# Kernel optimization log

Measured on AMD Instinct MI355X. Metric: run time of the kernel, lower is better.

Reference implementation:

```python
import jax, jax.numpy as jnp
import numpy as np

EPS = 1e-8  # RMSNormMultiHead default eps (forward passes self.eps)


def rms_norm_multihead(x, weight):
    # x: (B, L, H, d); normalize over last dim in float32, then scale per (H, d)
    x32 = x.astype(jnp.float32)
    normed = x32 * jax.lax.rsqrt(jnp.mean(x32 * x32, axis=-1, keepdims=True) + EPS)
    return normed.astype(x.dtype) * weight


def setup_inputs() -> dict:
    key = jax.random.key(0)
    k0, k1, k2 = jax.random.split(key, 3)
    B, L, D, H = 2, 1024, 1024, 16
    d = D // H
    X = jax.random.normal(k0, (B, L, D), dtype=jnp.float32)
    Wq = jax.random.normal(k1, (D, D), dtype=jnp.float32) * 0.02  # q_proj weight (out, in)
    Wv = jax.random.normal(k2, (D, D), dtype=jnp.float32) * 0.02  # v_proj weight (out, in)
    q_norm_w = jnp.ones((H, d), dtype=jnp.float32)
    v_norm_w = jnp.ones((H, d), dtype=jnp.float32)
    return {"X": X, "Wq": Wq, "Wv": Wv, "q_norm_w": q_norm_w, "v_norm_w": v_norm_w}


def reference(X, Wq, Wv, q_norm_w, v_norm_w):
    B, L, D = X.shape
    H, d = q_norm_w.shape
    K = X.reshape(B, L, H, d)
    Q = rms_norm_multihead((X @ Wq.T).reshape(B, L, H, d), q_norm_w)
    V = rms_norm_multihead((X @ Wv.T).reshape(B, L, H, d), v_norm_w)
    # cumulative outer-product KV state: (B, L, H, d, e)
    W = jnp.cumsum(jnp.einsum('blhd,blhe->blhde', K, V), axis=1)
    out = jnp.einsum('blhd,blhde->blhe', Q, W).reshape(B, L, D)
    return out
```

## Files before the change

### kernel.cpp

```cpp
#include <hip/hip_runtime.h>

#define BB 2
#define LL 1024
#define DD 1024
#define HH 16
#define NC 16
#define EPSF 1e-8f

typedef __attribute__((ext_vector_type(8))) short bf16x8;
typedef __attribute__((ext_vector_type(4))) float f32x4;
typedef unsigned short u16;

static __device__ inline u16 f2bf(float f) {
    unsigned int u = __builtin_bit_cast(unsigned int, f);
    u += 0x7fff + ((u >> 16) & 1);
    return (u16)(u >> 16);
}

static __device__ inline void gload_lds16(const u16* g, u16* l) {
    __builtin_amdgcn_global_load_lds((const __attribute__((address_space(1))) void*)g,
                                     (__attribute__((address_space(3))) void*)l, 16, 0, 0);
}

__global__ __launch_bounds__(256) void cvt_k(const float* __restrict__ X,
                                             const float* __restrict__ Wq,
                                             const float* __restrict__ Wv,
                                             u16* __restrict__ Xb,
                                             u16* __restrict__ Wqb,
                                             u16* __restrict__ Wvb)
{
    int i = (blockIdx.x * 256 + threadIdx.x) * 4;
    const float* s; u16* d; int off;
    if (i < 2*1024*1024)      { s = X;  d = Xb;  off = i; }
    else if (i < 3*1024*1024) { s = Wq; d = Wqb; off = i - 2*1024*1024; }
    else                      { s = Wv; d = Wvb; off = i - 3*1024*1024; }
    float4 v = *(const float4*)(s + off);
    ushort4 o;
    o.x = f2bf(v.x); o.y = f2bf(v.y); o.z = f2bf(v.z); o.w = f2bf(v.w);
    *(ushort4*)(d + off) = o;
}

__global__ __launch_bounds__(256) void gemm_fused(const u16* __restrict__ Xb,
                                                  const u16* __restrict__ Wqb,
                                                  const u16* __restrict__ Wvb,
                                                  const float* __restrict__ qw,
                                                  const float* __restrict__ vw,
                                                  u16* __restrict__ Qb,
                                                  u16* __restrict__ Vb)
{
    const int K = DD, N = DD;
    const u16* W = blockIdx.z ? Wvb : Wqb;
    const float* nw = blockIdx.z ? vw : qw;
    u16* Y = blockIdx.z ? Vb : Qb;
    __shared__ u16 As0[128 * 32], As1[128 * 32];
    __shared__ u16 Bs0[64 * 32],  Bs1[64 * 32];

    const int tid = threadIdx.x, w = tid >> 6, lane = tid & 63;
    const int quad = lane >> 4, l16 = lane & 15;
    const int m0 = blockIdx.y * 128, n0 = blockIdx.x * 64;
    const int lrow = lane >> 2, lcol = (lane & 3) * 8;

    const u16* gA0 = Xb + (size_t)(m0 + w*16 + lrow) * K + lcol;
    const u16* gA1 = gA0 + (size_t)64 * K;
    const u16* gB0 = W + (size_t)(n0 + w*16 + lrow) * K + lcol;
    u16* lA0_0 = &As0[(w*16) * 32];      u16* lA0_1 = &As1[(w*16) * 32];
    u16* lA1_0 = &As0[(64 + w*16) * 32]; u16* lA1_1 = &As1[(64 + w*16) * 32];
    u16* lB0_0 = &Bs0[(w*16) * 32];      u16* lB0_1 = &Bs1[(w*16) * 32];

    f32x4 acc[2][4] = {};
    for (int k0 = 0; k0 < K; k0 += 64) {
        gload_lds16(gA0 + k0,      lA0_0);
        gload_lds16(gA0 + k0 + 32, lA0_1);
        gload_lds16(gA1 + k0,      lA1_0);
        gload_lds16(gA1 + k0 + 32, lA1_1);
        gload_lds16(gB0 + k0,      lB0_0);
        gload_lds16(gB0 + k0 + 32, lB0_1);
        __syncthreads();
        #pragma unroll
        for (int hh = 0; hh < 2; ++hh) {
            const u16* Ah = hh ? As1 : As0;
            const u16* Bh = hh ? Bs1 : Bs0;
            bf16x8 af[2], bfr[4];
            #pragma unroll
            for (int i = 0; i < 2; ++i)
                af[i] = *(const bf16x8*)&Ah[(w*32 + i*16 + l16) * 32 + quad*8];
            #pragma unroll
            for (int j = 0; j < 4; ++j)
                bfr[j] = *(const bf16x8*)&Bh[(j*16 + l16) * 32 + quad*8];
            #pragma unroll
            for (int i = 0; i < 2; ++i)
                #pragma unroll
                for (int j = 0; j < 4; ++j)
                    acc[i][j] = __builtin_amdgcn_mfma_f32_16x16x32_bf16(af[i], bfr[j], acc[i][j], 0, 0, 0);
        }
        __syncthreads();
    }

    float wv[4];
    #pragma unroll
    for (int j = 0; j < 4; ++j) wv[j] = nw[n0 + j*16 + l16];
    #pragma unroll
    for (int i = 0; i < 2; ++i) {
        float ss[4];
        #pragma unroll
        for (int r = 0; r < 4; ++r) {
            float s = 0.f;
            #pragma unroll
            for (int j = 0; j < 4; ++j) s += acc[i][j][r] * acc[i][j][r];
            ss[r] = s;
        }
        #pragma unroll
        for (int off = 1; off < 16; off <<= 1)
            #pragma unroll
            for (int r = 0; r < 4; ++r) ss[r] += __shfl_xor(ss[r], off, 64);
        float sc[4];
        #pragma unroll
        for (int r = 0; r < 4; ++r) sc[r] = rsqrtf(ss[r] * (1.f/64.f) + EPSF);
        #pragma unroll
        for (int r = 0; r < 4; ++r) {
            u16* yp = Y + (size_t)(m0 + w*32 + i*16 + quad*4 + r) * N + n0;
            #pragma unroll
            for (int j = 0; j < 4; ++j)
                yp[j*16 + l16] = f2bf(acc[i][j][r] * sc[r] * wv[j]);
        }
    }
}

__global__ __launch_bounds__(256) void kv_scan(const u16* __restrict__ Xb,
                                               const u16* __restrict__ Vb,
                                               u16* __restrict__ S)
{
    const int t = blockIdx.x & 3, bh = blockIdx.x >> 2;
    const int et = t & 1, dt = t >> 1;
    const int h = bh & 15, b = bh >> 4;
    __shared__ u16 Kt[2][32][72];
    __shared__ u16 Vt[2][32][72];
    const int tid = threadIdx.x, w = tid >> 6, lane = tid & 63;
    const int quad = lane >> 4, l16 = lane & 15;
    const int esub = (w & 1) * 16, dsub = (w >> 1) * 16;
    const int half = tid >> 7, hrow = (tid & 127) >> 1, hq = tid & 1;
    const u16* gsrc = (half ? Vb : Xb) + (size_t)(b*LL + hrow) * DD
                      + h*64 + (half ? et : dt) * 32 + hq*16;
    u16 (*Tb)[32][72] = half ? Vt : Kt;
    ushort4 rr[4];

    auto loadc = [&](int c) {
        const u16* p = gsrc + (size_t)c * 64 * DD;
        rr[0] = *(const ushort4*)(p);      rr[1] = *(const ushort4*)(p + 4);
        rr[2] = *(const ushort4*)(p + 8);  rr[3] = *(const ushort4*)(p + 12);
    };
    auto writec = [&](int buf) {
        #pragma unroll
        for (int i = 0; i < 16; ++i)
            Tb[buf][hq*16 + i][hrow] = ((const u16*)rr)[i];
    };

    loadc(0); writec(0); loadc(1);
    __syncthreads();
    f32x4 acc = {};
    for (int c = 0; c < NC; ++c) {
        const int cur = c & 1;
        if (c + 1 < NC) writec(1 - cur);
        if (c + 2 < NC) loadc(c + 2);
        u16* Sp = S + (((size_t)(bh*NC + c)) << 12) + t*1024 + w*256;
        #pragma unroll
        for (int r = 0; r < 4; ++r) Sp[r*64 + lane] = f2bf(acc[r]);
        #pragma unroll
        for (int k0 = 0; k0 < 64; k0 += 32) {
            bf16x8 av = *(const bf16x8*)&Vt[cur][esub + l16][k0 + quad*8];
            bf16x8 bv = *(const bf16x8*)&Kt[cur][dsub + l16][k0 + quad*8];
            acc = __builtin_amdgcn_mfma_f32_16x16x32_bf16(av, bv, acc, 0, 0, 0);
        }
        __syncthreads();
    }
}

__global__ __launch_bounds__(256) void out_k(const u16* __restrict__ Xb,
                                             const u16* __restrict__ Qb,
                                             const u16* __restrict__ Vb,
                                             const u16* __restrict__ S,
                                             float* __restrict__ out)
{
    const int c = blockIdx.x & 15, bh = blockIdx.x >> 4;
    const int h = bh & 15, b = bh >> 4;
    __shared__ u16 Qs[64][72];
    __shared__ u16 Ks[64][72];
    __shared__ u16 Vt[64][72];
    __shared__ u16 St[64][72];
    const int tid = threadIdx.x;
    {
        const int row = tid >> 2, q = tid & 3;
        size_t gbase = (size_t)(b*LL + c*64 + row) * DD + h*64 + q*16;
        u16 vv[16];
        #pragma unroll
        for (int i = 0; i < 16; i += 4) {
            *(ushort4*)&Qs[row][q*16 + i] = *(const ushort4*)(Qb + gbase + i);
            *(ushort4*)&Ks[row][q*16 + i] = *(const ushort4*)(Xb + gbase + i);
            *(ushort4*)&vv[i] = *(const ushort4*)(Vb + gbase + i);
        }
        #pragma unroll
        for (int i = 0; i < 16; ++i)
            Vt[q*16 + i][row] = vv[i];
        const u16* Sc = S + (((size_t)(bh*NC + c)) << 12);
        #pragma unroll
        for (int j = 0; j < 4; ++j) {
            int f = (tid + j*256) * 4;
            ushort4 sv = *(const ushort4*)(Sc + f);
            int tt = f >> 10, ww = (f >> 8) & 3, rr_ = (f >> 6) & 3, ln = f & 63;
            int e = (tt & 1)*32 + (ww & 1)*16 + (ln >> 4)*4 + rr_;
            int d = (tt >> 1)*32 + ((ww >> 1) & 1)*16 + (ln & 15);
            *(ushort4*)&St[e][d] = sv;
        }
    }
    __syncthreads();
    const int w = tid >> 6, lane = tid & 63, quad = lane >> 4, l16 = lane & 15;
    const int mo = (w & 1) * 32, no = (w >> 1) * 32;

    f32x4 pacc[2][2] = {};
    #pragma unroll
    for (int k0 = 0; k0 < 64; k0 += 32) {
        bf16x8 aq[2], bk[2];
        #pragma unroll
        for (int i = 0; i < 2; ++i)
            aq[i] = *(const bf16x8*)&Qs[mo + i*16 + l16][k0 + quad*8];
        #pragma unroll
        for (int j = 0; j < 2; ++j)
            bk[j] = *(const bf16x8*)&Ks[no + j*16 + l16][k0 + quad*8];
        #pragma unroll
        for (int i = 0; i < 2; ++i)
            #pragma unroll
            for (int j = 0; j < 2; ++j)
                pacc[i][j] = __builtin_amdgcn_mfma_f32_16x16x32_bf16(aq[i], bk[j], pacc[i][j], 0, 0, 0);
    }
    __syncthreads();
    #pragma unroll
    for (int i = 0; i < 2; ++i)
        #pragma unroll
        for (int j = 0; j < 2; ++j)
            #pragma unroll
            for (int r = 0; r < 4; ++r) {
                int l  = mo + i*16 + quad*4 + r;
                int lp = no + j*16 + l16;
                Ks[l][lp] = (lp <= l) ? f2bf(pacc[i][j][r]) : (u16)0;
            }
    __syncthreads();

    f32x4 acc[2][2] = {};
    #pragma unroll
    for (int k0 = 0; k0 < 64; k0 += 32) {
        bf16x8 a1[2], b1[2], a2[2], b2[2];
        #pragma unroll
        for (int i = 0; i < 2; ++i) {
            a1[i] = *(const bf16x8*)&Ks[mo + i*16 + l16][k0 + quad*8];
            a2[i] = *(const bf16x8*)&Qs[mo + i*16 + l16][k0 + quad*8];
        }
        #pragma unroll
        for (int j = 0; j < 2; ++j) {
            b1[j] = *(const bf16x8*)&Vt[no + j*16 + l16][k0 + quad*8];
            b2[j] = *(const bf16x8*)&St[no + j*16 + l16][k0 + quad*8];
        }
        #pragma unroll
        for (int i = 0; i < 2; ++i)
            #pragma unroll
            for (int j = 0; j < 2; ++j) {
                acc[i][j] = __builtin_amdgcn_mfma_f32_16x16x32_bf16(a1[i], b1[j], acc[i][j], 0, 0, 0);
                acc[i][j] = __builtin_amdgcn_mfma_f32_16x16x32_bf16(a2[i], b2[j], acc[i][j], 0, 0, 0);
            }
    }
    float* op = out + (size_t)(b*LL + c*64) * DD + h*64;
    #pragma unroll
    for (int i = 0; i < 2; ++i)
        #pragma unroll
        for (int j = 0; j < 2; ++j)
            #pragma unroll
            for (int r = 0; r < 4; ++r)
                op[(size_t)(mo + i*16 + quad*4 + r) * DD + no + j*16 + l16] = acc[i][j][r];
}

extern "C" void kernel_launch(void* const* d_in, const int* in_sizes, int n_in,
                              void* d_out, int out_size, void* d_ws, size_t ws_size,
                              hipStream_t stream) {
    const float* X  = (const float*)d_in[0];
    const float* Wq = (const float*)d_in[1];
    const float* Wv = (const float*)d_in[2];
    const float* qw = (const float*)d_in[3];
    const float* vw = (const float*)d_in[4];
    float* out = (float*)d_out;

    u16* Xb  = (u16*)d_ws;
    u16* Wqb = Xb  + (size_t)2*1024*1024;
    u16* Wvb = Wqb + (size_t)1024*1024;
    u16* Qb  = Wvb + (size_t)1024*1024;
    u16* Vb  = Qb  + (size_t)2*1024*1024;
    u16* S   = Vb  + (size_t)2*1024*1024;

    cvt_k<<<4096, 256, 0, stream>>>(X, Wq, Wv, Xb, Wqb, Wvb);
    gemm_fused<<<dim3(16, 16, 2), 256, 0, stream>>>(Xb, Wqb, Wvb, qw, vw, Qb, Vb);
    kv_scan<<<128, 256, 0, stream>>>(Xb, Vb, S);
    out_k<<<BB*HH*NC, 256, 0, stream>>>(Xb, Qb, Vb, S, out);
}
```

Before: 106.2 us.

## Fuse all stages into one cooperative persistent kernel with chunk-parallel KV scan

Replaces the four separate launches (convert, fused GEMM+RMSNorm, KV scan, output) with a single cooperative kernel of 512 blocks that separates the phases with grid.sync. The sequential per-head KV scan is restructured into chunk-local outer-product sums computed in parallel, followed by a separate exclusive prefix pass over the 16 chunks. This targets launch overhead and the serial dependency in the old 128-block scan. In exchange it pays for grid-wide barriers, an extra global read/write of the state buffer, and requires all 512 blocks to be co-resident.

```diff
diff --git a/kernel.cpp b/kernel.cpp
--- a/kernel.cpp
+++ b/kernel.cpp
@@ -1,4 +1,7 @@
 #include <hip/hip_runtime.h>
+#include <hip/hip_cooperative_groups.h>
+
+namespace cg = cooperative_groups;
 
 #define BB 2
 #define LL 1024
@@ -10,271 +13,287 @@
 typedef __attribute__((ext_vector_type(8))) short bf16x8;
 typedef __attribute__((ext_vector_type(4))) float f32x4;
 typedef unsigned short u16;
+typedef u16 (*tile_t)[72];
 
 static __device__ inline u16 f2bf(float f) {
     unsigned int u = __builtin_bit_cast(unsigned int, f);
     u += 0x7fff + ((u >> 16) & 1);
     return (u16)(u >> 16);
 }
-
+static __device__ inline float bf2f(u16 v) {
+    unsigned int u = ((unsigned int)v) << 16;
+    return __builtin_bit_cast(float, u);
+}
 static __device__ inline void gload_lds16(const u16* g, u16* l) {
     __builtin_amdgcn_global_load_lds((const __attribute__((address_space(1))) void*)g,
                                      (__attribute__((address_space(3))) void*)l, 16, 0, 0);
 }
 
-__global__ __launch_bounds__(256) void cvt_k(const float* __restrict__ X,
-                                             const float* __restrict__ Wq,
-                                             const float* __restrict__ Wv,
-                                             u16* __restrict__ Xb,
-                                             u16* __restrict__ Wqb,
-                                             u16* __restrict__ Wvb)
+__global__ __launch_bounds__(256, 2) void fused_all(
+    const float* __restrict__ X, const float* __restrict__ Wq,
+    const float* __restrict__ Wv, const float* __restrict__ qw,
+    const float* __restrict__ vw,
+    u16* __restrict__ Xb, u16* __restrict__ Wqb, u16* __restrict__ Wvb,
+    u16* __restrict__ Qb, u16* __restrict__ Vb, u16* __restrict__ S,
+    float* __restrict__ out)
 {
-    int i = (blockIdx.x * 256 + threadIdx.x) * 4;
-    const float* s; u16* d; int off;
-    if (i < 2*1024*1024)      { s = X;  d = Xb;  off = i; }
-    else if (i < 3*1024*1024) { s = Wq; d = Wqb; off = i - 2*1024*1024; }
-    else                      { s = Wv; d = Wvb; off = i - 3*1024*1024; }
-    float4 v = *(const float4*)(s + off);
-    ushort4 o;
-    o.x = f2bf(v.x); o.y = f2bf(v.y); o.z = f2bf(v.z); o.w = f2bf(v.w);
-    *(ushort4*)(d + off) = o;
-}
-
-__global__ __launch_bounds__(256) void gemm_fused(const u16* __restrict__ Xb,
-                                                  const u16* __restrict__ Wqb,
-                                                  const u16* __restrict__ Wvb,
-                                                  const float* __restrict__ qw,
-                                                  const float* __restrict__ vw,
-                                                  u16* __restrict__ Qb,
-                                                  u16* __restrict__ Vb)
-{
-    const int K = DD, N = DD;
-    const u16* W = blockIdx.z ? Wvb : Wqb;
-    const float* nw = blockIdx.z ? vw : qw;
-    u16* Y = blockIdx.z ? Vb : Qb;
-    __shared__ u16 As0[128 * 32], As1[128 * 32];
-    __shared__ u16 Bs0[64 * 32],  Bs1[64 * 32];
-
-    const int tid = threadIdx.x, w = tid >> 6, lane = tid & 63;
+    cg::grid_group grid = cg::this_grid();
+    __shared__ u16 smem[18432];
+
+    const int tid = threadIdx.x, bid = blockIdx.x;
+    const int w = tid >> 6, lane = tid & 63;
     const int quad = lane >> 4, l16 = lane & 15;
-    const int m0 = blockIdx.y * 128, n0 = blockIdx.x * 64;
-    const int lrow = lane >> 2, lcol = (lane & 3) * 8;
-
-    const u16* gA0 = Xb + (size_t)(m0 + w*16 + lrow) * K + lcol;
-    const u16* gA1 = gA0 + (size_t)64 * K;
-    const u16* gB0 = W + (size_t)(n0 + w*16 + lrow) * K + lcol;
-    u16* lA0_0 = &As0[(w*16) * 32];      u16* lA0_1 = &As1[(w*16) * 32];
-    u16* lA1_0 = &As0[(64 + w*16) * 32]; u16* lA1_1 = &As1[(64 + w*16) * 32];
-    u16* lB0_0 = &Bs0[(w*16) * 32];      u16* lB0_1 = &Bs1[(w*16) * 32];
-
-    f32x4 acc[2][4] = {};
-    for (int k0 = 0; k0 < K; k0 += 64) {
-        gload_lds16(gA0 + k0,      lA0_0);
-        gload_lds16(gA0 + k0 + 32, lA0_1);
-        gload_lds16(gA1 + k0,      lA1_0);
-        gload_lds16(gA1 + k0 + 32, lA1_1);
-        gload_lds16(gB0 + k0,      lB0_0);
-        gload_lds16(gB0 + k0 + 32, lB0_1);
+
+    {
+        int i0 = (bid * 256 + tid) * 4;
+        #pragma unroll
+        for (int p = 0; p < 8; ++p) {
+            int i = i0 + p * 524288;
+            const float* s; u16* d; int off;
+            if (i < 2*1024*1024)      { s = X;  d = Xb;  off = i; }
+            else if (i < 3*1024*1024) { s = Wq; d = Wqb; off = i - 2*1024*1024; }
+            else                      { s = Wv; d = Wvb; off = i - 3*1024*1024; }
+            float4 v = *(const float4*)(s + off);
+            ushort4 o;
+            o.x = f2bf(v.x); o.y = f2bf(v.y); o.z = f2bf(v.z); o.w = f2bf(v.w);
+            *(ushort4*)(d + off) = o;
+        }
+    }
+    grid.sync();
+
+    {
+        const int z = bid >> 8, rem = bid & 255;
+        const int n0 = (rem & 15) * 64, m0 = (rem >> 4) * 128;
+        const u16* Wb = z ? Wvb : Wqb;
+        const float* nw = z ? vw : qw;
+        u16* Y = z ? Vb : Qb;
+        u16* As0 = smem;
+        u16* As1 = smem + 4096;
+        u16* Bs0 = smem + 8192;
+        u16* Bs1 = smem + 10240;
+
+        const int lrow = lane >> 2, lcol = (lane & 3) * 8;
+        const u16* gA0 = Xb + (size_t)(m0 + w*16 + lrow) * DD + lcol;
+        const u16* gA1 = gA0 + (size_t)64 * DD;
+        const u16* gB0 = Wb + (size_t)(n0 + w*16 + lrow) * DD + lcol;
+        u16* lA0_0 = &As0[(w*16) * 32];      u16* lA0_1 = &As1[(w*16) * 32];
+        u16* lA1_0 = &As0[(64 + w*16) * 32]; u16* lA1_1 = &As1[(64 + w*16) * 32];
+        u16* lB0_0 = &Bs0[(w*16) * 32];      u16* lB0_1 = &Bs1[(w*16) * 32];
+
+        f32x4 acc[2][4] = {};
+        for (int k0 = 0; k0 < DD; k0 += 64) {
+            gload_lds16(gA0 + k0,      lA0_0);
+            gload_lds16(gA0 + k0 + 32, lA0_1);
+            gload_lds16(gA1 + k0,      lA1_0);
+            gload_lds16(gA1 + k0 + 32, lA1_1);
+            gload_lds16(gB0 + k0,      lB0_0);
+            gload_lds16(gB0 + k0 + 32, lB0_1);
+            __syncthreads();
+            #pragma unroll
+            for (int hh = 0; hh < 2; ++hh) {
+                const u16* Ah = hh ? As1 : As0;
+                const u16* Bh = hh ? Bs1 : Bs0;
+                bf16x8 af[2], bfr[4];
+                #pragma unroll
+                for (int i = 0; i < 2; ++i)
+                    af[i] = *(const bf16x8*)&Ah[(w*32 + i*16 + l16) * 32 + quad*8];
+                #pragma unroll
+                for (int j = 0; j < 4; ++j)
+                    bfr[j] = *(const bf16x8*)&Bh[(j*16 + l16) * 32 + quad*8];
+                #pragma unroll
+                for (int i = 0; i < 2; ++i)
+                    #pragma unroll
+                    for (int j = 0; j < 4; ++j)
+                        acc[i][j] = __builtin_amdgcn_mfma_f32_16x16x32_bf16(af[i], bfr[j], acc[i][j], 0, 0, 0);
+            }
+            __syncthreads();
+        }
+        float wv4[4];
+        #pragma unroll
+        for (int j = 0; j < 4; ++j) wv4[j] = nw[n0 + j*16 + l16];
+        #pragma unroll
+        for (int i = 0; i < 2; ++i) {
+            float ss[4];
+            #pragma unroll
+            for (int r = 0; r < 4; ++r) {
+                float s = 0.f;
+                #pragma unroll
+                for (int j = 0; j < 4; ++j) s += acc[i][j][r] * acc[i][j][r];
+                ss[r] = s;
+            }
+            #pragma unroll
+            for (int off = 1; off < 16; off <<= 1)
+                #pragma unroll
+                for (int r = 0; r < 4; ++r) ss[r] += __shfl_xor(ss[r], off, 64);
+            float sc[4];
+            #pragma unroll
+            for (int r = 0; r < 4; ++r) sc[r] = rsqrtf(ss[r] * (1.f/64.f) + EPSF);
+            #pragma unroll
+            for (int r = 0; r < 4; ++r) {
+                u16* yp = Y + (size_t)(m0 + w*32 + i*16 + quad*4 + r) * DD + n0;
+                #pragma unroll
+                for (int j = 0; j < 4; ++j)
+                    yp[j*16 + l16] = f2bf(acc[i][j][r] * sc[r] * wv4[j]);
+            }
+        }
+    }
+    grid.sync();
+
+    {
+        const int bh = bid >> 4, c = bid & 15;
+        const int h = bh & 15, b = bh >> 4;
+        tile_t Kt = (tile_t)smem;
+        tile_t Vt = (tile_t)(smem + 4608);
+        {
+            const int row = tid >> 2, q = tid & 3;
+            size_t gbase = (size_t)(b*LL + c*64 + row) * DD + h*64 + q*16;
+            u16 kk[16], vv[16];
+            #pragma unroll
+            for (int i = 0; i < 16; i += 4) {
+                *(ushort4*)&kk[i] = *(const ushort4*)(Xb + gbase + i);
+                *(ushort4*)&vv[i] = *(const ushort4*)(Vb + gbase + i);
+            }
+            #pragma unroll
+            for (int i = 0; i < 16; ++i) {
+                Kt[q*16 + i][row] = kk[i];
+                Vt[q*16 + i][row] = vv[i];
+            }
+        }
         __syncthreads();
-        #pragma unroll
-        for (int hh = 0; hh < 2; ++hh) {
-            const u16* Ah = hh ? As1 : As0;
-            const u16* Bh = hh ? Bs1 : Bs0;
-            bf16x8 af[2], bfr[4];
-            #pragma unroll
-            for (int i = 0; i < 2; ++i)
-                af[i] = *(const bf16x8*)&Ah[(w*32 + i*16 + l16) * 32 + quad*8];
-            #pragma unroll
-            for (int j = 0; j < 4; ++j)
-                bfr[j] = *(const bf16x8*)&Bh[(j*16 + l16) * 32 + quad*8];
-            #pragma unroll
-            for (int i = 0; i < 2; ++i)
-                #pragma unroll
-                for (int j = 0; j < 4; ++j)
-                    acc[i][j] = __builtin_amdgcn_mfma_f32_16x16x32_bf16(af[i], bfr[j], acc[i][j], 0, 0, 0);
+        const int me = (w & 1) * 32, nd = (w >> 1) * 32;
+        f32x4 acc[2][2] = {};
+        #pragma unroll
+        for (int k0 = 0; k0 < 64; k0 += 32) {
+            bf16x8 av[2], bv[2];
+            #pragma unroll
+            for (int i = 0; i < 2; ++i)
+                av[i] = *(const bf16x8*)&Vt[me + i*16 + l16][k0 + quad*8];
+            #pragma unroll
+            for (int j = 0; j < 2; ++j)
+                bv[j] = *(const bf16x8*)&Kt[nd + j*16 + l16][k0 + quad*8];
+            #pragma unroll
+            for (int i = 0; i < 2; ++i)
+                #pragma unroll
+                for (int j = 0; j < 2; ++j)
+                    acc[i][j] = __builtin_amdgcn_mfma_f32_16x16x32_bf16(av[i], bv[j], acc[i][j], 0, 0, 0);
+        }
+        u16* Sp = S + ((size_t)bid << 12) + w*1024;
+        #pragma unroll
+        for (int i = 0; i < 2; ++i)
+            #pragma unroll
+            for (int j = 0; j < 2; ++j)
+                #pragma unroll
+                for (int r = 0; r < 4; ++r)
+                    Sp[(i*2 + j)*256 + r*64 + lane] = f2bf(acc[i][j][r]);
+    }
+    grid.sync();
+
+    {
+        const int gid = bid * 256 + tid;
+        const int bh = gid >> 12, pos = gid & 4095;
+        u16* base = S + (size_t)bh * 65536 + pos;
+        float run = 0.f;
+        #pragma unroll
+        for (int c = 0; c < NC; ++c) {
+            float v = bf2f(base[c * 4096]);
+            base[c * 4096] = f2bf(run);
+            run += v;
+        }
+    }
+    grid.sync();
+
+    {
+        const int c = bid & 15, bh = bid >> 4;
+        const int h = bh & 15, b = bh >> 4;
+        tile_t Qs = (tile_t)smem;
+        tile_t Ks = (tile_t)(smem + 4608);
+        tile_t Vt = (tile_t)(smem + 9216);
+        tile_t St = (tile_t)(smem + 13824);
+        {
+            const int row = tid >> 2, q = tid & 3;
+            size_t gbase = (size_t)(b*LL + c*64 + row) * DD + h*64 + q*16;
+            u16 vv[16];
+            #pragma unroll
+            for (int i = 0; i < 16; i += 4) {
+                *(ushort4*)&Qs[row][q*16 + i] = *(const ushort4*)(Qb + gbase + i);
+                *(ushort4*)&Ks[row][q*16 + i] = *(const ushort4*)(Xb + gbase + i);
+                *(ushort4*)&vv[i] = *(const ushort4*)(Vb + gbase + i);
+            }
+            #pragma unroll
+            for (int i = 0; i < 16; ++i)
+                Vt[q*16 + i][row] = vv[i];
+            const u16* Sc = S + ((size_t)bid << 12);
+            #pragma unroll
+            for (int jj = 0; jj < 4; ++jj) {
+                int f = (tid + jj*256) * 4;
+                ushort4 sv = *(const ushort4*)(Sc + f);
+                int w_ = f >> 10, fij = (f >> 8) & 3, r_ = (f >> 6) & 3, ln = f & 63;
+                int e = (w_ & 1)*32 + (fij >> 1)*16 + (ln >> 4)*4 + r_;
+                int d = (w_ >> 1)*32 + (fij & 1)*16 + (ln & 15);
+                *(ushort4*)&St[e][d] = sv;
+            }
         }
         __syncthreads();
-    }
-
-    float wv[4];
-    #pragma unroll
-    for (int j = 0; j < 4; ++j) wv[j] = nw[n0 + j*16 + l16];
-    #pragma unroll
-    for (int i = 0; i < 2; ++i) {
-        float ss[4];
-        #pragma unroll
-        for (int r = 0; r < 4; ++r) {
-            float s = 0.f;
-            #pragma unroll
-            for (int j = 0; j < 4; ++j) s += acc[i][j][r] * acc[i][j][r];
-            ss[r] = s;
-        }
-        #pragma unroll
-        for (int off = 1; off < 16; off <<= 1)
-            #pragma unroll
-            for (int r = 0; r < 4; ++r) ss[r] += __shfl_xor(ss[r], off, 64);
-        float sc[4];
-        #pragma unroll
-        for (int r = 0; r < 4; ++r) sc[r] = rsqrtf(ss[r] * (1.f/64.f) + EPSF);
-        #pragma unroll
-        for (int r = 0; r < 4; ++r) {
-            u16* yp = Y + (size_t)(m0 + w*32 + i*16 + quad*4 + r) * N + n0;
-            #pragma unroll
-            for (int j = 0; j < 4; ++j)
-                yp[j*16 + l16] = f2bf(acc[i][j][r] * sc[r] * wv[j]);
-        }
-    }
-}
-
-__global__ __launch_bounds__(256) void kv_scan(const u16* __restrict__ Xb,
-                                               const u16* __restrict__ Vb,
-                                               u16* __restrict__ S)
-{
-    const int t = blockIdx.x & 3, bh = blockIdx.x >> 2;
-    const int et = t & 1, dt = t >> 1;
-    const int h = bh & 15, b = bh >> 4;
-    __shared__ u16 Kt[2][32][72];
-    __shared__ u16 Vt[2][32][72];
-    const int tid = threadIdx.x, w = tid >> 6, lane = tid & 63;
-    const int quad = lane >> 4, l16 = lane & 15;
-    const int esub = (w & 1) * 16, dsub = (w >> 1) * 16;
-    const int half = tid >> 7, hrow = (tid & 127) >> 1, hq = tid & 1;
-    const u16* gsrc = (half ? Vb : Xb) + (size_t)(b*LL + hrow) * DD
-                      + h*64 + (half ? et : dt) * 32 + hq*16;
-    u16 (*Tb)[32][72] = half ? Vt : Kt;
-    ushort4 rr[4];
-
-    auto loadc = [&](int c) {
-        const u16* p = gsrc + (size_t)c * 64 * DD;
-        rr[0] = *(const ushort4*)(p);      rr[1] = *(const ushort4*)(p + 4);
-        rr[2] = *(const ushort4*)(p + 8);  rr[3] = *(const ushort4*)(p + 12);
-    };
-    auto writec = [&](int buf) {
-        #pragma unroll
-        for (int i = 0; i < 16; ++i)
-            Tb[buf][hq*16 + i][hrow] = ((const u16*)rr)[i];
-    };
-
-    loadc(0); writec(0); loadc(1);
-    __syncthreads();
-    f32x4 acc = {};
-    for (int c = 0; c < NC; ++c) {
-        const int cur = c & 1;
-        if (c + 1 < NC) writec(1 - cur);
-        if (c + 2 < NC) loadc(c + 2);
-        u16* Sp = S + (((size_t)(bh*NC + c)) << 12) + t*1024 + w*256;
-        #pragma unroll
-        for (int r = 0; r < 4; ++r) Sp[r*64 + lane] = f2bf(acc[r]);
+        const int mo = (w & 1) * 32, no = (w >> 1) * 32;
+        f32x4 pacc[2][2] = {};
         #pragma unroll
         for (int k0 = 0; k0 < 64; k0 += 32) {
-            bf16x8 av = *(const bf16x8*)&Vt[cur][esub + l16][k0 + quad*8];
-            bf16x8 bv = *(const bf16x8*)&Kt[cur][dsub + l16][k0 + quad*8];
-            acc = __builtin_amdgcn_mfma_f32_16x16x32_bf16(av, bv, acc, 0, 0, 0);
+            bf16x8 aq[2], bk[2];
+            #pragma unroll
+            for (int i = 0; i < 2; ++i)
+                aq[i] = *(const bf16x8*)&Qs[mo + i*16 + l16][k0 + quad*8];
+            #pragma unroll
+            for (int j = 0; j < 2; ++j)
+                bk[j] = *(const bf16x8*)&Ks[no + j*16 + l16][k0 + quad*8];
+            #pragma unroll
+            for (int i = 0; i < 2; ++i)
+                #pragma unroll
+                for (int j = 0; j < 2; ++j)
+                    pacc[i][j] = __builtin_amdgcn_mfma_f32_16x16x32_bf16(aq[i], bk[j], pacc[i][j], 0, 0, 0);
         }
         __syncthreads();
-    }
-}
-
-__global__ __launch_bounds__(256) void out_k(const u16* __restrict__ Xb,
-                                             const u16* __restrict__ Qb,
-                                             const u16* __restrict__ Vb,
-                                             const u16* __restrict__ S,
-                                             float* __restrict__ out)
-{
-    const int c = blockIdx.x & 15, bh = blockIdx.x >> 4;
-    const int h = bh & 15, b = bh >> 4;
-    __shared__ u16 Qs[64][72];
-    __shared__ u16 Ks[64][72];
-    __shared__ u16 Vt[64][72];
-    __shared__ u16 St[64][72];
-    const int tid = threadIdx.x;
-    {
-        const int row = tid >> 2, q = tid & 3;
-        size_t gbase = (size_t)(b*LL + c*64 + row) * DD + h*64 + q*16;
-        u16 vv[16];
-        #pragma unroll
-        for (int i = 0; i < 16; i += 4) {
-            *(ushort4*)&Qs[row][q*16 + i] = *(const ushort4*)(Qb + gbase + i);
-            *(ushort4*)&Ks[row][q*16 + i] = *(const ushort4*)(Xb + gbase + i);
-            *(ushort4*)&vv[i] = *(const ushort4*)(Vb + gbase + i);
-        }
-        #pragma unroll
-        for (int i = 0; i < 16; ++i)
-            Vt[q*16 + i][row] = vv[i];
-        const u16* Sc = S + (((size_t)(bh*NC + c)) << 12);
-        #pragma unroll
-        for (int j = 0; j < 4; ++j) {
-            int f = (tid + j*256) * 4;
-            ushort4 sv = *(const ushort4*)(Sc + f);
-            int tt = f >> 10, ww = (f >> 8) & 3, rr_ = (f >> 6) & 3, ln = f & 63;
-            int e = (tt & 1)*32 + (ww & 1)*16 + (ln >> 4)*4 + rr_;
-            int d = (tt >> 1)*32 + ((ww >> 1) & 1)*16 + (ln & 15);
-            *(ushort4*)&St[e][d] = sv;
-        }
-    }
-    __syncthreads();
-    const int w = tid >> 6, lane = tid & 63, quad = lane >> 4, l16 = lane & 15;
-    const int mo = (w & 1) * 32, no = (w >> 1) * 32;
-
-    f32x4 pacc[2][2] = {};
-    #pragma unroll
-    for (int k0 = 0; k0 < 64; k0 += 32) {
-        bf16x8 aq[2], bk[2];
         #pragma unroll
         for (int i = 0; i < 2; ++i)
-            aq[i] = *(const bf16x8*)&Qs[mo + i*16 + l16][k0 + quad*8];
-        #pragma unroll
-        for (int j = 0; j < 2; ++j)
-            bk[j] = *(const bf16x8*)&Ks[no + j*16 + l16][k0 + quad*8];
+            #pragma unroll
+            for (int j = 0; j < 2; ++j)
+                #pragma unroll
+                for (int r = 0; r < 4; ++r) {
+                    int l  = mo + i*16 + quad*4 + r;
+                    int lp = no + j*16 + l16;
+                    Ks[l][lp] = (lp <= l) ? f2bf(pacc[i][j][r]) : (u16)0;
+                }
+        __syncthreads();
+        f32x4 acc[2][2] = {};
+        #pragma unroll
+        for (int k0 = 0; k0 < 64; k0 += 32) {
+            bf16x8 a1[2], b1[2], a2[2], b2[2];
+            #pragma unroll
+            for (int i = 0; i < 2; ++i) {
+                a1[i] = *(const bf16x8*)&Ks[mo + i*16 + l16][k0 + quad*8];
+                a2[i] = *(const bf16x8*)&Qs[mo + i*16 + l16][k0 + quad*8];
+            }
+            #pragma unroll
+            for (int j = 0; j < 2; ++j) {
+                b1[j] = *(const bf16x8*)&Vt[no + j*16 + l16][k0 + quad*8];
+                b2[j] = *(const bf16x8*)&St[no + j*16 + l16][k0 + quad*8];
+            }
+            #pragma unroll
+            for (int i = 0; i < 2; ++i)
+                #pragma unroll
+                for (int j = 0; j < 2; ++j) {
+                    acc[i][j] = __builtin_amdgcn_mfma_f32_16x16x32_bf16(a1[i], b1[j], acc[i][j], 0, 0, 0);
+                    acc[i][j] = __builtin_amdgcn_mfma_f32_16x16x32_bf16(a2[i], b2[j], acc[i][j], 0, 0, 0);
+                }
+        }
+        float* op = out + (size_t)(b*LL + c*64) * DD + h*64;
         #pragma unroll
         for (int i = 0; i < 2; ++i)
             #pragma unroll
             for (int j = 0; j < 2; ++j)
-                pacc[i][j] = __builtin_amdgcn_mfma_f32_16x16x32_bf16(aq[i], bk[j], pacc[i][j], 0, 0, 0);
-    }
-    __syncthreads();
-    #pragma unroll
-    for (int i = 0; i < 2; ++i)
-        #pragma unroll
-        for (int j = 0; j < 2; ++j)
-            #pragma unroll
-            for (int r = 0; r < 4; ++r) {
-                int l  = mo + i*16 + quad*4 + r;
-                int lp = no + j*16 + l16;
-                Ks[l][lp] = (lp <= l) ? f2bf(pacc[i][j][r]) : (u16)0;
-            }
-    __syncthreads();
-
-    f32x4 acc[2][2] = {};
-    #pragma unroll
-    for (int k0 = 0; k0 < 64; k0 += 32) {
-        bf16x8 a1[2], b1[2], a2[2], b2[2];
-        #pragma unroll
-        for (int i = 0; i < 2; ++i) {
-            a1[i] = *(const bf16x8*)&Ks[mo + i*16 + l16][k0 + quad*8];
-            a2[i] = *(const bf16x8*)&Qs[mo + i*16 + l16][k0 + quad*8];
-        }
-        #pragma unroll
-        for (int j = 0; j < 2; ++j) {
-            b1[j] = *(const bf16x8*)&Vt[no + j*16 + l16][k0 + quad*8];
-            b2[j] = *(const bf16x8*)&St[no + j*16 + l16][k0 + quad*8];
-        }
-        #pragma unroll
-        for (int i = 0; i < 2; ++i)
-            #pragma unroll
-            for (int j = 0; j < 2; ++j) {
-                acc[i][j] = __builtin_amdgcn_mfma_f32_16x16x32_bf16(a1[i], b1[j], acc[i][j], 0, 0, 0);
-                acc[i][j] = __builtin_amdgcn_mfma_f32_16x16x32_bf16(a2[i], b2[j], acc[i][j], 0, 0, 0);
-            }
-    }
-    float* op = out + (size_t)(b*LL + c*64) * DD + h*64;
-    #pragma unroll
-    for (int i = 0; i < 2; ++i)
-        #pragma unroll
-        for (int j = 0; j < 2; ++j)
-            #pragma unroll
-            for (int r = 0; r < 4; ++r)
-                op[(size_t)(mo + i*16 + quad*4 + r) * DD + no + j*16 + l16] = acc[i][j][r];
+                #pragma unroll
+                for (int r = 0; r < 4; ++r)
+                    op[(size_t)(mo + i*16 + quad*4 + r) * DD + no + j*16 + l16] = acc[i][j][r];
+    }
 }
 
 extern "C" void kernel_launch(void* const* d_in, const int* in_sizes, int n_in,
@@ -294,8 +313,9 @@
     u16* Vb  = Qb  + (size_t)2*1024*1024;
     u16* S   = Vb  + (size_t)2*1024*1024;
 
-    cvt_k<<<4096, 256, 0, stream>>>(X, Wq, Wv, Xb, Wqb, Wvb);
-    gemm_fused<<<dim3(16, 16, 2), 256, 0, stream>>>(Xb, Wqb, Wvb, qw, vw, Qb, Vb);
-    kv_scan<<<128, 256, 0, stream>>>(Xb, Vb, S);
-    out_k<<<BB*HH*NC, 256, 0, stream>>>(Xb, Qb, Vb, S, out);
-}
+    void* args[] = { (void*)&X, (void*)&Wq, (void*)&Wv, (void*)&qw, (void*)&vw,
+                     (void*)&Xb, (void*)&Wqb, (void*)&Wvb, (void*)&Qb, (void*)&Vb,
+                     (void*)&S, (void*)&out };
+    hipLaunchCooperativeKernel((void*)fused_all, dim3(512), dim3(256),
+                               args, 0, stream);
+}
```

After: 351.9 us. +231.3%, slower.

## Fuse KV prefix-state scan into output kernel, recomputing state per chunk

Applied to the files above, without the earlier changes.

Drops the separate kv_scan kernel and its bf16 state buffer. Each output block now rebuilds its chunk's prefix KV state by summing outer products over all earlier chunks, then does the intra-chunk and inter-chunk matmuls. Chunk indices are reversed so the blocks with the most prefix work start first. This removes one launch and the state-buffer write and read, but adds redundant work that grows quadratically with chunk count, and load imbalance across blocks. Precision also changes: the prefix state stays in fp32 accumulators until one final bf16 rounding.

```diff
diff --git a/kernel.cpp b/kernel.cpp
--- a/kernel.cpp
+++ b/kernel.cpp
@@ -96,9 +96,9 @@
         __syncthreads();
     }
 
-    float wv[4];
-    #pragma unroll
-    for (int j = 0; j < 4; ++j) wv[j] = nw[n0 + j*16 + l16];
+    float wv4[4];
+    #pragma unroll
+    for (int j = 0; j < 4; ++j) wv4[j] = nw[n0 + j*16 + l16];
     #pragma unroll
     for (int i = 0; i < 2; ++i) {
         float ss[4];
@@ -121,101 +121,99 @@
             u16* yp = Y + (size_t)(m0 + w*32 + i*16 + quad*4 + r) * N + n0;
             #pragma unroll
             for (int j = 0; j < 4; ++j)
-                yp[j*16 + l16] = f2bf(acc[i][j][r] * sc[r] * wv[j]);
-        }
-    }
-}
-
-__global__ __launch_bounds__(256) void kv_scan(const u16* __restrict__ Xb,
-                                               const u16* __restrict__ Vb,
-                                               u16* __restrict__ S)
+                yp[j*16 + l16] = f2bf(acc[i][j][r] * sc[r] * wv4[j]);
+        }
+    }
+}
+
+__global__ __launch_bounds__(256) void out_mega(const u16* __restrict__ Xb,
+                                                const u16* __restrict__ Qb,
+                                                const u16* __restrict__ Vb,
+                                                float* __restrict__ out)
 {
-    const int t = blockIdx.x & 3, bh = blockIdx.x >> 2;
-    const int et = t & 1, dt = t >> 1;
-    const int h = bh & 15, b = bh >> 4;
-    __shared__ u16 Kt[2][32][72];
-    __shared__ u16 Vt[2][32][72];
-    const int tid = threadIdx.x, w = tid >> 6, lane = tid & 63;
-    const int quad = lane >> 4, l16 = lane & 15;
-    const int esub = (w & 1) * 16, dsub = (w >> 1) * 16;
-    const int half = tid >> 7, hrow = (tid & 127) >> 1, hq = tid & 1;
-    const u16* gsrc = (half ? Vb : Xb) + (size_t)(b*LL + hrow) * DD
-                      + h*64 + (half ? et : dt) * 32 + hq*16;
-    u16 (*Tb)[32][72] = half ? Vt : Kt;
-    ushort4 rr[4];
-
-    auto loadc = [&](int c) {
-        const u16* p = gsrc + (size_t)c * 64 * DD;
-        rr[0] = *(const ushort4*)(p);      rr[1] = *(const ushort4*)(p + 4);
-        rr[2] = *(const ushort4*)(p + 8);  rr[3] = *(const ushort4*)(p + 12);
-    };
-    auto writec = [&](int buf) {
-        #pragma unroll
-        for (int i = 0; i < 16; ++i)
-            Tb[buf][hq*16 + i][hrow] = ((const u16*)rr)[i];
-    };
-
-    loadc(0); writec(0); loadc(1);
-    __syncthreads();
-    f32x4 acc = {};
-    for (int c = 0; c < NC; ++c) {
-        const int cur = c & 1;
-        if (c + 1 < NC) writec(1 - cur);
-        if (c + 2 < NC) loadc(c + 2);
-        u16* Sp = S + (((size_t)(bh*NC + c)) << 12) + t*1024 + w*256;
-        #pragma unroll
-        for (int r = 0; r < 4; ++r) Sp[r*64 + lane] = f2bf(acc[r]);
-        #pragma unroll
-        for (int k0 = 0; k0 < 64; k0 += 32) {
-            bf16x8 av = *(const bf16x8*)&Vt[cur][esub + l16][k0 + quad*8];
-            bf16x8 bv = *(const bf16x8*)&Kt[cur][dsub + l16][k0 + quad*8];
-            acc = __builtin_amdgcn_mfma_f32_16x16x32_bf16(av, bv, acc, 0, 0, 0);
-        }
-        __syncthreads();
-    }
-}
-
-__global__ __launch_bounds__(256) void out_k(const u16* __restrict__ Xb,
-                                             const u16* __restrict__ Qb,
-                                             const u16* __restrict__ Vb,
-                                             const u16* __restrict__ S,
-                                             float* __restrict__ out)
-{
-    const int c = blockIdx.x & 15, bh = blockIdx.x >> 4;
+    const int c = 15 - (blockIdx.x & 15);
+    const int bh = blockIdx.x >> 4;
     const int h = bh & 15, b = bh >> 4;
     __shared__ u16 Qs[64][72];
-    __shared__ u16 Ks[64][72];
+    __shared__ u16 Ko[64][72];
+    __shared__ u16 Vo[64][72];
+    __shared__ u16 St[64][72];
+    __shared__ u16 Kt[64][72];
     __shared__ u16 Vt[64][72];
-    __shared__ u16 St[64][72];
     const int tid = threadIdx.x;
+    const int row = tid >> 2, q = tid & 3;
+    const int w = tid >> 6, lane = tid & 63, quad = lane >> 4, l16 = lane & 15;
+
     {
-        const int row = tid >> 2, q = tid & 3;
         size_t gbase = (size_t)(b*LL + c*64 + row) * DD + h*64 + q*16;
         u16 vv[16];
         #pragma unroll
         for (int i = 0; i < 16; i += 4) {
             *(ushort4*)&Qs[row][q*16 + i] = *(const ushort4*)(Qb + gbase + i);
-            *(ushort4*)&Ks[row][q*16 + i] = *(const ushort4*)(Xb + gbase + i);
+            *(ushort4*)&Ko[row][q*16 + i] = *(const ushort4*)(Xb + gbase + i);
             *(ushort4*)&vv[i] = *(const ushort4*)(Vb + gbase + i);
         }
         #pragma unroll
         for (int i = 0; i < 16; ++i)
-            Vt[q*16 + i][row] = vv[i];
-        const u16* Sc = S + (((size_t)(bh*NC + c)) << 12);
-        #pragma unroll
-        for (int j = 0; j < 4; ++j) {
-            int f = (tid + j*256) * 4;
-            ushort4 sv = *(const ushort4*)(Sc + f);
-            int tt = f >> 10, ww = (f >> 8) & 3, rr_ = (f >> 6) & 3, ln = f & 63;
-            int e = (tt & 1)*32 + (ww & 1)*16 + (ln >> 4)*4 + rr_;
-            int d = (tt >> 1)*32 + ((ww >> 1) & 1)*16 + (ln & 15);
-            *(ushort4*)&St[e][d] = sv;
+            Vo[q*16 + i][row] = vv[i];
+    }
+
+    const int we = (w & 1) * 32, wd = (w >> 1) * 32;
+    f32x4 sacc[2][2] = {};
+    const u16* gK = Xb + (size_t)(b*LL + row) * DD + h*64 + q*16;
+    const u16* gV = Vb + (size_t)(b*LL + row) * DD + h*64 + q*16;
+    ushort4 kr[4], vr[4];
+    if (c > 0) {
+        #pragma unroll
+        for (int i = 0; i < 4; ++i) {
+            kr[i] = *(const ushort4*)(gK + i*4);
+            vr[i] = *(const ushort4*)(gV + i*4);
         }
     }
     __syncthreads();
-    const int w = tid >> 6, lane = tid & 63, quad = lane >> 4, l16 = lane & 15;
+    for (int cp = 0; cp < c; ++cp) {
+        #pragma unroll
+        for (int i = 0; i < 16; ++i) {
+            Kt[q*16 + i][row] = ((const u16*)kr)[i];
+            Vt[q*16 + i][row] = ((const u16*)vr)[i];
+        }
+        __syncthreads();
+        if (cp + 1 < c) {
+            const u16* nK = gK + (size_t)(cp+1)*64*DD;
+            const u16* nV = gV + (size_t)(cp+1)*64*DD;
+            #pragma unroll
+            for (int i = 0; i < 4; ++i) {
+                kr[i] = *(const ushort4*)(nK + i*4);
+                vr[i] = *(const ushort4*)(nV + i*4);
+            }
+        }
+        #pragma unroll
+        for (int k0 = 0; k0 < 64; k0 += 32) {
+            bf16x8 av[2], bv[2];
+            #pragma unroll
+            for (int i = 0; i < 2; ++i)
+                av[i] = *(const bf16x8*)&Vt[we + i*16 + l16][k0 + quad*8];
+            #pragma unroll
+            for (int j = 0; j < 2; ++j)
+                bv[j] = *(const bf16x8*)&Kt[wd + j*16 + l16][k0 + quad*8];
+            #pragma unroll
+            for (int i = 0; i < 2; ++i)
+                #pragma unroll
+                for (int j = 0; j < 2; ++j)
+                    sacc[i][j] = __builtin_amdgcn_mfma_f32_16x16x32_bf16(av[i], bv[j], sacc[i][j], 0, 0, 0);
+        }
+        __syncthreads();
+    }
+
+    #pragma unroll
+    for (int i = 0; i < 2; ++i)
+        #pragma unroll
+        for (int j = 0; j < 2; ++j)
+            #pragma unroll
+            for (int r = 0; r < 4; ++r)
+                St[we + i*16 + quad*4 + r][wd + j*16 + l16] = f2bf(sacc[i][j][r]);
+
     const int mo = (w & 1) * 32, no = (w >> 1) * 32;
-
     f32x4 pacc[2][2] = {};
     #pragma unroll
     for (int k0 = 0; k0 < 64; k0 += 32) {
@@ -225,7 +223,7 @@
             aq[i] = *(const bf16x8*)&Qs[mo + i*16 + l16][k0 + quad*8];
         #pragma unroll
         for (int j = 0; j < 2; ++j)
-            bk[j] = *(const bf16x8*)&Ks[no + j*16 + l16][k0 + quad*8];
+            bk[j] = *(const bf16x8*)&Ko[no + j*16 + l16][k0 + quad*8];
         #pragma unroll
         for (int i = 0; i < 2; ++i)
             #pragma unroll
@@ -241,7 +239,7 @@
             for (int r = 0; r < 4; ++r) {
                 int l  = mo + i*16 + quad*4 + r;
                 int lp = no + j*16 + l16;
-                Ks[l][lp] = (lp <= l) ? f2bf(pacc[i][j][r]) : (u16)0;
+                Ko[l][lp] = (lp <= l) ? f2bf(pacc[i][j][r]) : (u16)0;
             }
     __syncthreads();
 
@@ -251,12 +249,12 @@
         bf16x8 a1[2], b1[2], a2[2], b2[2];
         #pragma unroll
         for (int i = 0; i < 2; ++i) {
-            a1[i] = *(const bf16x8*)&Ks[mo + i*16 + l16][k0 + quad*8];
+            a1[i] = *(const bf16x8*)&Ko[mo + i*16 + l16][k0 + quad*8];
             a2[i] = *(const bf16x8*)&Qs[mo + i*16 + l16][k0 + quad*8];
         }
         #pragma unroll
         for (int j = 0; j < 2; ++j) {
-            b1[j] = *(const bf16x8*)&Vt[no + j*16 + l16][k0 + quad*8];
+            b1[j] = *(const bf16x8*)&Vo[no + j*16 + l16][k0 + quad*8];
             b2[j] = *(const bf16x8*)&St[no + j*16 + l16][k0 + quad*8];
         }
         #pragma unroll
@@ -292,10 +290,8 @@
     u16* Wvb = Wqb + (size_t)1024*1024;
     u16* Qb  = Wvb + (size_t)1024*1024;
     u16* Vb  = Qb  + (size_t)2*1024*1024;
-    u16* S   = Vb  + (size_t)2*1024*1024;
 
     cvt_k<<<4096, 256, 0, stream>>>(X, Wq, Wv, Xb, Wqb, Wvb);
     gemm_fused<<<dim3(16, 16, 2), 256, 0, stream>>>(Xb, Wqb, Wvb, qw, vw, Qb, Vb);
-    kv_scan<<<128, 256, 0, stream>>>(Xb, Vb, S);
-    out_k<<<BB*HH*NC, 256, 0, stream>>>(Xb, Qb, Vb, S, out);
-}
+    out_mega<<<BB*HH*NC, 256, 0, stream>>>(Xb, Qb, Vb, out);
+}
```

Result: slower. 112.8 us (+6.2%).
